# Performance work log

Measured on AMD Instinct MI355X. Metric: run time of the kernel, lower is better.

Reference implementation:

```python
import jax, jax.numpy as jnp
import numpy as np

B = 32768
INPUT_DIM = 128
MAX_DIM = 1024          # max_dynamic_reservoir_dim (pre-allocated)
ACTIVE = 512            # current_reservoir_size (runtime-active prefix)
LEAK = 0.2              # initial leak_rate
THRESH = 0.5            # initial spike_threshold


def setup_inputs() -> dict:
    key = jax.random.key(0)
    k = jax.random.split(key, 5)
    inputs = jax.random.normal(k[0], (B, INPUT_DIM), dtype=jnp.float32)
    prev_state = jax.random.normal(k[1], (B, MAX_DIM), dtype=jnp.float32)
    # Weights initialized like tf RandomNormal(stddev=0.1), pre-allocated to max dim
    W_res = 0.1 * jax.random.normal(k[2], (MAX_DIM, MAX_DIM), dtype=jnp.float32)
    W_in = 0.1 * jax.random.normal(k[3], (MAX_DIM, INPUT_DIM), dtype=jnp.float32)
    W_gate = 0.1 * jax.random.normal(k[4], (3 * MAX_DIM, INPUT_DIM), dtype=jnp.float32)
    # Trainable per-neuron params, initialized to inverse-sigmoid / inverse-softplus of initial values
    leak_rate_param = jnp.full((MAX_DIM,), np.log(LEAK / (1.0 - LEAK)), dtype=jnp.float32)
    spike_threshold_param = jnp.full((MAX_DIM,), np.log(np.expm1(THRESH)), dtype=jnp.float32)
    return {
        'inputs': inputs,
        'prev_state': prev_state,
        'W_res': W_res,
        'W_in': W_in,
        'W_gate': W_gate,
        'leak_rate_param': leak_rate_param,
        'spike_threshold_param': spike_threshold_param,
        'active_size': ACTIVE,
    }


def reference(inputs, prev_state, W_res, W_in, W_gate, leak_rate_param,
              spike_threshold_param, active_size):
    A = active_size
    max_dim = prev_state.shape[1]
    prev = prev_state[:, :A]                                   # [B, A]
    leak = jax.nn.sigmoid(leak_rate_param[:A])                 # [A]
    thr = jax.nn.softplus(spike_threshold_param[:A])           # [A]
    input_part = inputs @ W_in[:A, :].T                        # [B, A]
    reservoir_part = prev @ W_res[:A, :A]                      # [B, A]
    gates = jax.nn.sigmoid(inputs @ W_gate[:3 * A, :].T)       # [B, 3A]
    i_gate, f_gate, o_gate = jnp.split(gates, 3, axis=-1)
    state = (1.0 - leak) * (f_gate * prev) + leak * jnp.tanh(i_gate * (input_part + reservoir_part))
    state = o_gate * state
    # Threshold-triggered spiking reset: subtract threshold where state exceeds it
    state = jnp.where(state > thr, state - thr, state)
    # Pad active state back to the full pre-allocated reservoir width
    return jnp.pad(state, ((0, 0), (0, max_dim - A)))
```

## Files before the change

kernel.cpp:

```cpp
#include <hip/hip_runtime.h>
#include <cmath>

#define NB   32768
#define DIN  128
#define DMAX 1024
#define A    512

typedef _Float16 half8 __attribute__((ext_vector_type(8)));
typedef float f32x4 __attribute__((ext_vector_type(4)));

#define WS_RES_H 0
#define WS_RES_L 262144
#define WS_PAN   524288

__global__ __launch_bounds__(256) void split_weights(
    const float* __restrict__ Wres, const float* __restrict__ Win,
    const float* __restrict__ Wg, _Float16* __restrict__ ws)
{
    int idx = blockIdx.x * 256 + threadIdx.x;
    if (idx < 262144) {
        int k = idx >> 9, j = idx & 511;
        float v = Wres[k * DMAX + j];
        _Float16 h = (_Float16)v;
        _Float16 l = (_Float16)(v - (float)h);
        int off = ((j >> 7) * 16 + (k >> 5)) * 4096 + (j & 127) * 32 + (k & 31);
        ws[WS_RES_H + off] = h;
        ws[WS_RES_L + off] = l;
    } else {
        int r = idx - 262144;
        int p = r >> 16;
        int q = r & 65535;
        int j = q >> 7, k = q & 127;
        float v = (p == 0) ? Win[j * DIN + k]
                           : Wg[((p - 1) * 512 + j) * DIN + k];
        _Float16 h = (_Float16)v;
        _Float16 l = (_Float16)(v - (float)h);
        int off = ((j >> 7) * 4 + (k >> 5)) * 4096 + (j & 127) * 32 + (k & 31);
        ws[WS_PAN + p * 131072 + off] = h;
        ws[WS_PAN + p * 131072 + 65536 + off] = l;
    }
}

__device__ __forceinline__ float sigm(float x) { return 1.0f / (1.0f + expf(-x)); }

__global__ __launch_bounds__(256, 2) void gser_mfma(
    const float* __restrict__ X,
    const float* __restrict__ P,
    const _Float16* __restrict__ ws,
    const float* __restrict__ lrp, const float* __restrict__ stp,
    float* __restrict__ out)
{
    __shared__ _Float16 Ah[128][40], Al[128][40], Bh[128][40], Bl[128][40];

    const int t    = threadIdx.x;
    const int lane = t & 63;
    const int w    = t >> 6;
    const int wm   = w & 1, wn = w >> 1;
    const int quad = lane >> 4, l16 = lane & 15;
    const int jb   = blockIdx.x;
    const int m0   = blockIdx.y * 128;
    const int j0   = jb * 128;

    const int sm = t >> 1;
    const int sk = (t & 1) * 16;

    auto stageA = [&](const float* src, int lda, int k0) {
        const float* p = src + (size_t)sm * lda + k0 + sk;
        float4 f0 = *(const float4*)(p);
        float4 f1 = *(const float4*)(p + 4);
        float4 f2 = *(const float4*)(p + 8);
        float4 f3 = *(const float4*)(p + 12);
        float fv[16] = {f0.x,f0.y,f0.z,f0.w, f1.x,f1.y,f1.z,f1.w,
                        f2.x,f2.y,f2.z,f2.w, f3.x,f3.y,f3.z,f3.w};
        half8 hh0, hh1, ll0, ll1;
#pragma unroll
        for (int i = 0; i < 8; ++i) {
            _Float16 h = (_Float16)fv[i];
            hh0[i] = h; ll0[i] = (_Float16)(fv[i] - (float)h);
        }
#pragma unroll
        for (int i = 0; i < 8; ++i) {
            _Float16 h = (_Float16)fv[8 + i];
            hh1[i] = h; ll1[i] = (_Float16)(fv[8 + i] - (float)h);
        }
        *(half8*)&Ah[sm][sk]     = hh0;
        *(half8*)&Ah[sm][sk + 8] = hh1;
        *(half8*)&Al[sm][sk]     = ll0;
        *(half8*)&Al[sm][sk + 8] = ll1;
    };

    auto stageB = [&](const _Float16* chH, const _Float16* chL) {
#pragma unroll
        for (int r = 0; r < 2; ++r) {
            int s  = t + r * 256;
            int bj = s >> 2, bk = (s & 3) * 8;
            *(half8*)&Bh[bj][bk] = *(const half8*)(chH + s * 8);
            *(half8*)&Bl[bj][bk] = *(const half8*)(chL + s * 8);
        }
    };

    auto mmac = [&](f32x4 (&C)[4][4]) {
        half8 fah[4], fal[4];
#pragma unroll
        for (int ms = 0; ms < 4; ++ms) {
            int row = wm * 64 + ms * 16 + l16;
            fah[ms] = *(const half8*)&Ah[row][quad * 8];
            fal[ms] = *(const half8*)&Al[row][quad * 8];
        }
#pragma unroll
        for (int js = 0; js < 4; ++js) {
            int col = wn * 64 + js * 16 + l16;
            half8 fbh = *(const half8*)&Bh[col][quad * 8];
            half8 fbl = *(const half8*)&Bl[col][quad * 8];
#pragma unroll
            for (int ms = 0; ms < 4; ++ms) {
                C[ms][js] = __builtin_amdgcn_mfma_f32_16x16x32_f16(fah[ms], fbh, C[ms][js], 0, 0, 0);
                C[ms][js] = __builtin_amdgcn_mfma_f32_16x16x32_f16(fah[ms], fbl, C[ms][js], 0, 0, 0);
                C[ms][js] = __builtin_amdgcn_mfma_f32_16x16x32_f16(fal[ms], fbh, C[ms][js], 0, 0, 0);
            }
        }
    };

    f32x4 accS[4][4];
#pragma unroll
    for (int i = 0; i < 4; ++i)
#pragma unroll
        for (int j = 0; j < 4; ++j)
            accS[i][j] = (f32x4){0.f, 0.f, 0.f, 0.f};

    const float* Pblk = P + (size_t)m0 * DMAX;
    for (int kc = 0; kc < 16; ++kc) {
        __syncthreads();
        stageA(Pblk, DMAX, kc * 32);
        const _Float16* ch = ws + WS_RES_H + (size_t)(jb * 16 + kc) * 4096;
        const _Float16* cl = ws + WS_RES_L + (size_t)(jb * 16 + kc) * 4096;
        stageB(ch, cl);
        __syncthreads();
        mmac(accS);
    }

    const float* Xblk = X + (size_t)m0 * DIN;
    for (int kc = 0; kc < 4; ++kc) {
        __syncthreads();
        stageA(Xblk, DIN, kc * 32);
        const _Float16* base = ws + WS_PAN + 0 * 131072;
        stageB(base + (size_t)(jb * 4 + kc) * 4096,
               base + 65536 + (size_t)(jb * 4 + kc) * 4096);
        __syncthreads();
        mmac(accS);
    }

    f32x4 accG[4][4];

#pragma unroll
    for (int i = 0; i < 4; ++i)
#pragma unroll
        for (int j = 0; j < 4; ++j)
            accG[i][j] = (f32x4){0.f, 0.f, 0.f, 0.f};
    for (int kc = 0; kc < 4; ++kc) {
        __syncthreads();
        stageA(Xblk, DIN, kc * 32);
        const _Float16* base = ws + WS_PAN + 1 * 131072;
        stageB(base + (size_t)(jb * 4 + kc) * 4096,
               base + 65536 + (size_t)(jb * 4 + kc) * 4096);
        __syncthreads();
        mmac(accG);
    }
#pragma unroll
    for (int ms = 0; ms < 4; ++ms)
#pragma unroll
        for (int js = 0; js < 4; ++js)
#pragma unroll
            for (int r = 0; r < 4; ++r)
                accS[ms][js][r] = tanhf(sigm(accG[ms][js][r]) * accS[ms][js][r]);

#pragma unroll
    for (int i = 0; i < 4; ++i)
#pragma unroll
        for (int j = 0; j < 4; ++j)
            accG[i][j] = (f32x4){0.f, 0.f, 0.f, 0.f};
    for (int kc = 0; kc < 4; ++kc) {
        __syncthreads();
        stageA(Xblk, DIN, kc * 32);
        const _Float16* base = ws + WS_PAN + 2 * 131072;
        stageB(base + (size_t)(jb * 4 + kc) * 4096,
               base + 65536 + (size_t)(jb * 4 + kc) * 4096);
        __syncthreads();
        mmac(accG);
    }
    {
        float lk[4];
#pragma unroll
        for (int js = 0; js < 4; ++js)
            lk[js] = sigm(lrp[j0 + wn * 64 + js * 16 + l16]);
#pragma unroll
        for (int ms = 0; ms < 4; ++ms)
#pragma unroll
            for (int r = 0; r < 4; ++r) {
                int row = m0 + wm * 64 + ms * 16 + quad * 4 + r;
#pragma unroll
                for (int js = 0; js < 4; ++js) {
                    int col = j0 + wn * 64 + js * 16 + l16;
                    float pv = P[(size_t)row * DMAX + col];
                    float fg = sigm(accG[ms][js][r]);
                    accS[ms][js][r] = (1.0f - lk[js]) * (fg * pv) + lk[js] * accS[ms][js][r];
                }
            }
    }

#pragma unroll
    for (int i = 0; i < 4; ++i)
#pragma unroll
        for (int j = 0; j < 4; ++j)
            accG[i][j] = (f32x4){0.f, 0.f, 0.f, 0.f};
    for (int kc = 0; kc < 4; ++kc) {
        __syncthreads();
        stageA(Xblk, DIN, kc * 32);
        const _Float16* base = ws + WS_PAN + 3 * 131072;
        stageB(base + (size_t)(jb * 4 + kc) * 4096,
               base + 65536 + (size_t)(jb * 4 + kc) * 4096);
        __syncthreads();
        mmac(accG);
    }
    {
        float thr[4];
#pragma unroll
        for (int js = 0; js < 4; ++js)
            thr[js] = log1pf(expf(stp[j0 + wn * 64 + js * 16 + l16]));
#pragma unroll
        for (int ms = 0; ms < 4; ++ms)
#pragma unroll
            for (int r = 0; r < 4; ++r) {
                int row = m0 + wm * 64 + ms * 16 + quad * 4 + r;
#pragma unroll
                for (int js = 0; js < 4; ++js) {
                    int col = j0 + wn * 64 + js * 16 + l16;
                    float st = sigm(accG[ms][js][r]) * accS[ms][js][r];
                    st = (st > thr[js]) ? (st - thr[js]) : st;
                    out[(size_t)row * DMAX + col] = st;
                }
            }
    }

#pragma unroll
    for (int i = 0; i < 16; ++i) {
        int s  = t + i * 256;
        int rr = s >> 5, c4 = s & 31;
        *(float4*)(out + (size_t)(m0 + rr) * DMAX + A + jb * 128 + c4 * 4) =
            (float4){0.f, 0.f, 0.f, 0.f};
    }
}

extern "C" void kernel_launch(void* const* d_in, const int* in_sizes, int n_in,
                              void* d_out, int out_size, void* d_ws, size_t ws_size,
                              hipStream_t stream) {
    const float* X    = (const float*)d_in[0];
    const float* P    = (const float*)d_in[1];
    const float* Wres = (const float*)d_in[2];
    const float* Win  = (const float*)d_in[3];
    const float* Wg   = (const float*)d_in[4];
    const float* lrp  = (const float*)d_in[5];
    const float* stp  = (const float*)d_in[6];
    float* out = (float*)d_out;
    _Float16* ws = (_Float16*)d_ws;

    hipLaunchKernelGGL(split_weights, dim3(2048), dim3(256), 0, stream,
                       Wres, Win, Wg, ws);
    hipLaunchKernelGGL(gser_mfma, dim3(4, 256), dim3(256), 0, stream,
                       X, P, ws, lrp, stp, out);
}
```

Baseline: 448.7 us.

## Pre-split activations to swizzled fp16 tiles and stream via global_load_lds double buffering

Adds a prep kernel that converts X and prev_state, along with the weights, into hi/lo fp16 tile layouts with an XOR swizzle in the workspace. A new main kernel then loads those tiles directly into LDS with global_load_lds and a double-buffered pipeline, and remaps blocks so neighbouring ones share tiles in cache. It also switches to fast exp-based sigmoid and tanh. This removes per-block fp32-to-fp16 conversion and register staging in the GEMM loop, at the cost of an extra full pass that reads and writes the activations. The new path runs only when the workspace is large enough; otherwise the old path is kept.

Measured after the change: 507.8 us. 13.2% more time.

```diff
diff --git a/kernel.cpp b/kernel.cpp
--- a/kernel.cpp
+++ b/kernel.cpp
@@ -12,6 +12,14 @@
 #define WS_RES_H 0
 #define WS_RES_L 262144
 #define WS_PAN   524288
+#define WS_X     1048576
+#define WS_X_LD  4194304
+#define WS_P     9437184
+#define WS_P_LD  16777216
+#define WS_NEED_BYTES 85983232ull
+
+#define SWZB(b) ((b) ^ ((((b) >> 6) & 7) << 4))
+__device__ __forceinline__ unsigned swzh(unsigned h) { return h ^ (((h >> 5) & 7u) << 3); }
 
 __global__ __launch_bounds__(256) void split_weights(
     const float* __restrict__ Wres, const float* __restrict__ Win,
@@ -44,8 +52,7 @@
 __device__ __forceinline__ float sigm(float x) { return 1.0f / (1.0f + expf(-x)); }
 
 __global__ __launch_bounds__(256, 2) void gser_mfma(
-    const float* __restrict__ X,
-    const float* __restrict__ P,
+    const float* __restrict__ X, const float* __restrict__ P,
     const _Float16* __restrict__ ws,
     const float* __restrict__ lrp, const float* __restrict__ stp,
     float* __restrict__ out)
@@ -236,6 +243,278 @@
                 for (int js = 0; js < 4; ++js) {
                     int col = j0 + wn * 64 + js * 16 + l16;
                     float st = sigm(accG[ms][js][r]) * accS[ms][js][r];
+                    st = (st > thr[js]) ? (st - thr[js]) : st;
+                    out[(size_t)row * DMAX + col] = st;
+                }
+            }
+    }
+
+#pragma unroll
+    for (int i = 0; i < 16; ++i) {
+        int s  = t + i * 256;
+        int rr = s >> 5, c4 = s & 31;
+        *(float4*)(out + (size_t)(m0 + rr) * DMAX + A + jb * 128 + c4 * 4) =
+            (float4){0.f, 0.f, 0.f, 0.f};
+    }
+}
+
+
+__global__ __launch_bounds__(256) void prep_full(
+    const float* __restrict__ X, const float* __restrict__ P,
+    const float* __restrict__ Wres, const float* __restrict__ Win,
+    const float* __restrict__ Wg, _Float16* __restrict__ ws)
+{
+    const int NRES = 32768;
+    const int NPAN = 32768;
+    const int NX   = 524288;
+    const int NTOT = NRES + NPAN + NX + 2097152;
+    for (int gi = blockIdx.x * 256 + threadIdx.x; gi < NTOT; gi += gridDim.x * 256) {
+        float v[8];
+        size_t dH, dL;
+        if (gi < NRES) {
+            int j = gi & 511, k0 = (gi >> 9) << 3;
+#pragma unroll
+            for (int i = 0; i < 8; ++i) v[i] = Wres[(size_t)(k0 + i) * DMAX + j];
+            unsigned off = (unsigned)((j >> 7) * 16 + (k0 >> 5)) * 4096u
+                         + swzh((unsigned)((j & 127) * 32 + (k0 & 31)));
+            dH = WS_RES_H + off; dL = WS_RES_L + off;
+        } else if (gi < NRES + NPAN) {
+            int r = gi - NRES;
+            int pj = r >> 4, k0 = (r & 15) << 3;
+            int p = pj >> 9, j = pj & 511;
+            const float* s = (p == 0) ? (Win + (size_t)j * DIN + k0)
+                                      : (Wg + (size_t)((p - 1) * 512 + j) * DIN + k0);
+            float4 f0 = *(const float4*)s, f1 = *(const float4*)(s + 4);
+            v[0] = f0.x; v[1] = f0.y; v[2] = f0.z; v[3] = f0.w;
+            v[4] = f1.x; v[5] = f1.y; v[6] = f1.z; v[7] = f1.w;
+            unsigned off = (unsigned)((j >> 7) * 4 + (k0 >> 5)) * 4096u
+                         + swzh((unsigned)((j & 127) * 32 + (k0 & 31)));
+            dH = WS_PAN + (size_t)p * 131072 + off; dL = dH + 65536;
+        } else if (gi < NRES + NPAN + NX) {
+            int r = gi - (NRES + NPAN);
+            int m = r >> 4, k0 = (r & 15) << 3;
+            const float* s = X + (size_t)m * DIN + k0;
+            float4 f0 = *(const float4*)s, f1 = *(const float4*)(s + 4);
+            v[0] = f0.x; v[1] = f0.y; v[2] = f0.z; v[3] = f0.w;
+            v[4] = f1.x; v[5] = f1.y; v[6] = f1.z; v[7] = f1.w;
+            unsigned off = (unsigned)((m >> 7) * 4 + (k0 >> 5)) * 4096u
+                         + swzh((unsigned)((m & 127) * 32 + (k0 & 31)));
+            dH = WS_X + off; dL = dH + WS_X_LD;
+        } else {
+            int r = gi - (NRES + NPAN + NX);
+            int m = r >> 6, k0 = (r & 63) << 3;
+            const float* s = P + (size_t)m * DMAX + k0;
+            float4 f0 = *(const float4*)s, f1 = *(const float4*)(s + 4);
+            v[0] = f0.x; v[1] = f0.y; v[2] = f0.z; v[3] = f0.w;
+            v[4] = f1.x; v[5] = f1.y; v[6] = f1.z; v[7] = f1.w;
+            unsigned off = (unsigned)((m >> 7) * 16 + (k0 >> 5)) * 4096u
+                         + swzh((unsigned)((m & 127) * 32 + (k0 & 31)));
+            dH = WS_P + off; dL = dH + WS_P_LD;
+        }
+        half8 hh, ll;
+#pragma unroll
+        for (int i = 0; i < 8; ++i) {
+            _Float16 h = (_Float16)v[i];
+            hh[i] = h;
+            ll[i] = (_Float16)(v[i] - (float)h);
+        }
+        *(half8*)(ws + dH) = hh;
+        *(half8*)(ws + dL) = ll;
+    }
+}
+
+__device__ __forceinline__ float fsigm(float x) { return 1.0f / (1.0f + __expf(-x)); }
+__device__ __forceinline__ float ftanh(float x) {
+    float e = __expf(-2.0f * fabsf(x));
+    float t = (1.0f - e) / (1.0f + e);
+    return (x < 0.0f) ? -t : t;
+}
+
+__device__ __forceinline__ void gl16(const _Float16* src, _Float16* dst) {
+    __builtin_amdgcn_global_load_lds(
+        (const __attribute__((address_space(1))) unsigned int*)src,
+        (__attribute__((address_space(3))) unsigned int*)dst, 16, 0, 0);
+}
+
+__global__ __launch_bounds__(256, 2) void gser2(
+    const float* __restrict__ X, const float* __restrict__ P,
+    const _Float16* __restrict__ ws,
+    const float* __restrict__ lrp, const float* __restrict__ stp,
+    float* __restrict__ out)
+{
+    __shared__ _Float16 lds[2][16384];
+
+    const int t    = threadIdx.x;
+    const int lane = t & 63;
+    const int w    = t >> 6;
+    const int wm   = w & 1, wn = w >> 1;
+    const int quad = lane >> 4, l16 = lane & 15;
+
+    const int id = blockIdx.x;
+    const int x8 = id & 7;
+    const int s8 = id >> 3;
+    const int jb = s8 & 3;
+    const int g  = (s8 >> 2) * 8 + x8;
+    const int m0 = g * 128;
+    const int j0 = jb * 128;
+
+    int aOff[4], bOff[4];
+#pragma unroll
+    for (int ms = 0; ms < 4; ++ms) {
+        int b = (wm * 64 + ms * 16 + l16) * 64 + quad * 16;
+        aOff[ms] = SWZB(b);
+    }
+#pragma unroll
+    for (int js = 0; js < 4; ++js) {
+        int b = (wn * 64 + js * 16 + l16) * 64 + quad * 16;
+        bOff[js] = SWZB(b);
+    }
+
+    const int so = w * 512 + lane * 8;
+    const int dd = w * 512;
+
+    auto stage = [&](int buf, int s) {
+        const _Float16 *aB, *bB;
+        unsigned aLd, bLd;
+        if (s < 16) {
+            aB = ws + WS_P + (size_t)(g * 16 + s) * 4096;      aLd = WS_P_LD;
+            bB = ws + WS_RES_H + (size_t)(jb * 16 + s) * 4096; bLd = 262144u;
+        } else {
+            int p = (s - 16) >> 2, kc = s & 3;
+            aB = ws + WS_X + (size_t)(g * 4 + kc) * 4096;      aLd = WS_X_LD;
+            bB = ws + WS_PAN + (size_t)p * 131072 + (size_t)(jb * 4 + kc) * 4096;
+            bLd = 65536u;
+        }
+        _Float16* l = &lds[buf][0];
+#pragma unroll
+        for (int i = 0; i < 2; ++i) {
+            gl16(aB + so + i * 2048,       l + dd + i * 2048);
+            gl16(aB + aLd + so + i * 2048, l + 4096  + dd + i * 2048);
+            gl16(bB + so + i * 2048,       l + 8192  + dd + i * 2048);
+            gl16(bB + bLd + so + i * 2048, l + 12288 + dd + i * 2048);
+        }
+    };
+
+    auto mmac = [&](int buf, f32x4 (&C)[4][4]) {
+        const char* base = (const char*)&lds[buf][0];
+        half8 fah[4], fal[4];
+#pragma unroll
+        for (int ms = 0; ms < 4; ++ms) {
+            fah[ms] = *(const half8*)(base + aOff[ms]);
+            fal[ms] = *(const half8*)(base + 8192 + aOff[ms]);
+        }
+#pragma unroll
+        for (int js = 0; js < 4; ++js) {
+            half8 fbh = *(const half8*)(base + 16384 + bOff[js]);
+            half8 fbl = *(const half8*)(base + 24576 + bOff[js]);
+#pragma unroll
+            for (int ms = 0; ms < 4; ++ms) {
+                C[ms][js] = __builtin_amdgcn_mfma_f32_16x16x32_f16(fah[ms], fbh, C[ms][js], 0, 0, 0);
+                C[ms][js] = __builtin_amdgcn_mfma_f32_16x16x32_f16(fah[ms], fbl, C[ms][js], 0, 0, 0);
+                C[ms][js] = __builtin_amdgcn_mfma_f32_16x16x32_f16(fal[ms], fbh, C[ms][js], 0, 0, 0);
+            }
+        }
+    };
+
+    f32x4 accS[4][4], accG[4][4];
+#pragma unroll
+    for (int i = 0; i < 4; ++i)
+#pragma unroll
+        for (int j = 0; j < 4; ++j)
+            accS[i][j] = (f32x4){0.f, 0.f, 0.f, 0.f};
+
+    int buf = 0;
+    stage(0, 0);
+    __syncthreads();
+
+    for (int s = 0; s < 16; ++s) {
+        stage(buf ^ 1, s + 1);
+        mmac(buf, accS);
+        __syncthreads();
+        buf ^= 1;
+    }
+    for (int s = 16; s < 20; ++s) {
+        stage(buf ^ 1, s + 1);
+        mmac(buf, accS);
+        __syncthreads();
+        buf ^= 1;
+    }
+
+#pragma unroll
+    for (int i = 0; i < 4; ++i)
+#pragma unroll
+        for (int j = 0; j < 4; ++j)
+            accG[i][j] = (f32x4){0.f, 0.f, 0.f, 0.f};
+    for (int s = 20; s < 24; ++s) {
+        stage(buf ^ 1, s + 1);
+        mmac(buf, accG);
+        __syncthreads();
+        buf ^= 1;
+    }
+#pragma unroll
+    for (int ms = 0; ms < 4; ++ms)
+#pragma unroll
+        for (int js = 0; js < 4; ++js)
+#pragma unroll
+            for (int r = 0; r < 4; ++r)
+                accS[ms][js][r] = ftanh(fsigm(accG[ms][js][r]) * accS[ms][js][r]);
+
+#pragma unroll
+    for (int i = 0; i < 4; ++i)
+#pragma unroll
+        for (int j = 0; j < 4; ++j)
+            accG[i][j] = (f32x4){0.f, 0.f, 0.f, 0.f};
+    for (int s = 24; s < 28; ++s) {
+        stage(buf ^ 1, s + 1);
+        mmac(buf, accG);
+        __syncthreads();
+        buf ^= 1;
+    }
+    {
+        float lk[4];
+#pragma unroll
+        for (int js = 0; js < 4; ++js)
+            lk[js] = fsigm(lrp[j0 + wn * 64 + js * 16 + l16]);
+#pragma unroll
+        for (int ms = 0; ms < 4; ++ms)
+#pragma unroll
+            for (int r = 0; r < 4; ++r) {
+                int row = m0 + wm * 64 + ms * 16 + quad * 4 + r;
+#pragma unroll
+                for (int js = 0; js < 4; ++js) {
+                    int col = j0 + wn * 64 + js * 16 + l16;
+                    float pv = P[(size_t)row * DMAX + col];
+                    float fg = fsigm(accG[ms][js][r]);
+                    accS[ms][js][r] = (1.0f - lk[js]) * (fg * pv) + lk[js] * accS[ms][js][r];
+                }
+            }
+    }
+
+#pragma unroll
+    for (int i = 0; i < 4; ++i)
+#pragma unroll
+        for (int j = 0; j < 4; ++j)
+            accG[i][j] = (f32x4){0.f, 0.f, 0.f, 0.f};
+    for (int s = 28; s < 32; ++s) {
+        if (s < 31) stage(buf ^ 1, s + 1);
+        mmac(buf, accG);
+        __syncthreads();
+        buf ^= 1;
+    }
+    {
+        float thr[4];
+#pragma unroll
+        for (int js = 0; js < 4; ++js)
+            thr[js] = log1pf(__expf(stp[j0 + wn * 64 + js * 16 + l16]));
+#pragma unroll
+        for (int ms = 0; ms < 4; ++ms)
+#pragma unroll
+            for (int r = 0; r < 4; ++r) {
+                int row = m0 + wm * 64 + ms * 16 + quad * 4 + r;
+#pragma unroll
+                for (int js = 0; js < 4; ++js) {
+                    int col = j0 + wn * 64 + js * 16 + l16;
+                    float st = fsigm(accG[ms][js][r]) * accS[ms][js][r];
                     st = (st > thr[js]) ? (st - thr[js]) : st;
                     out[(size_t)row * DMAX + col] = st;
                 }
@@ -264,8 +543,15 @@
     float* out = (float*)d_out;
     _Float16* ws = (_Float16*)d_ws;
 
-    hipLaunchKernelGGL(split_weights, dim3(2048), dim3(256), 0, stream,
-                       Wres, Win, Wg, ws);
-    hipLaunchKernelGGL(gser_mfma, dim3(4, 256), dim3(256), 0, stream,
-                       X, P, ws, lrp, stp, out);
-}
+    if (ws_size >= WS_NEED_BYTES) {
+        hipLaunchKernelGGL(prep_full, dim3(10496), dim3(256), 0, stream,
+                           X, P, Wres, Win, Wg, ws);
+        hipLaunchKernelGGL(gser2, dim3(1024), dim3(256), 0, stream,
+                           X, P, ws, lrp, stp, out);
+    } else {
+        hipLaunchKernelGGL(split_weights, dim3(2048), dim3(256), 0, stream,
+                           Wres, Win, Wg, ws);
+        hipLaunchKernelGGL(gser_mfma, dim3(4, 256), dim3(256), 0, stream,
+                           X, P, ws, lrp, stp, out);
+    }
+}
```

## Double-buffer LDS with async global-to-LDS loads, swizzled layout, fast math

Applied to the files above, without the earlier changes.

Moves the main kernel to a double-buffered LDS pipeline. The weight tiles go straight from global memory into LDS with global_load_lds, while the next A tile is loaded into registers and converted during the current MFMA step, leaving one barrier per step. Weights are pre-swizzled in a rewritten prep kernel so LDS fragment reads avoid bank conflicts. Block indices are remapped for L2 locality, and expf/tanhf are replaced with __expf-based approximations. The fast math may lose some accuracy, and the dependence on the swizzle and the async-load layout adds correctness risk.

Measured after the change: 498.5 us. +11.1%, slower.

```diff
diff --git a/kernel.cpp b/kernel.cpp
--- a/kernel.cpp
+++ b/kernel.cpp
@@ -13,105 +13,161 @@
 #define WS_RES_L 262144
 #define WS_PAN   524288
 
-__global__ __launch_bounds__(256) void split_weights(
+#define SWZB(b) ((b) ^ ((((b) >> 6) & 7) << 4))
+__device__ __forceinline__ unsigned swzh(unsigned h) { return h ^ (((h >> 5) & 7u) << 3); }
+
+__device__ __forceinline__ float fsigm(float x) { return 1.0f / (1.0f + __expf(-x)); }
+__device__ __forceinline__ float ftanh(float x) {
+    float e = __expf(-2.0f * fabsf(x));
+    float t = (1.0f - e) / (1.0f + e);
+    return (x < 0.0f) ? -t : t;
+}
+
+__device__ __forceinline__ void gl16(const _Float16* src, _Float16* dst) {
+    __builtin_amdgcn_global_load_lds(
+        (const __attribute__((address_space(1))) unsigned int*)src,
+        (__attribute__((address_space(3))) unsigned int*)dst, 16, 0, 0);
+}
+
+__global__ __launch_bounds__(256) void prep_w(
     const float* __restrict__ Wres, const float* __restrict__ Win,
     const float* __restrict__ Wg, _Float16* __restrict__ ws)
 {
-    int idx = blockIdx.x * 256 + threadIdx.x;
-    if (idx < 262144) {
-        int k = idx >> 9, j = idx & 511;
-        float v = Wres[k * DMAX + j];
-        _Float16 h = (_Float16)v;
-        _Float16 l = (_Float16)(v - (float)h);
-        int off = ((j >> 7) * 16 + (k >> 5)) * 4096 + (j & 127) * 32 + (k & 31);
-        ws[WS_RES_H + off] = h;
-        ws[WS_RES_L + off] = l;
+    int tid = blockIdx.x * 256 + threadIdx.x;
+    float v[32];
+    size_t dH, dL;
+    int j = tid & 127;
+    if (tid < 8192) {
+        int c = tid >> 7;
+        int jbb = c >> 4, kc = c & 15;
+        int col = jbb * 128 + j;
+#pragma unroll
+        for (int i = 0; i < 32; ++i)
+            v[i] = Wres[(size_t)(kc * 32 + i) * DMAX + col];
+        dH = WS_RES_H + (size_t)c * 4096;
+        dL = WS_RES_L + (size_t)c * 4096;
     } else {
-        int r = idx - 262144;
-        int p = r >> 16;
-        int q = r & 65535;
-        int j = q >> 7, k = q & 127;
-        float v = (p == 0) ? Win[j * DIN + k]
-                           : Wg[((p - 1) * 512 + j) * DIN + k];
-        _Float16 h = (_Float16)v;
-        _Float16 l = (_Float16)(v - (float)h);
-        int off = ((j >> 7) * 4 + (k >> 5)) * 4096 + (j & 127) * 32 + (k & 31);
-        ws[WS_PAN + p * 131072 + off] = h;
-        ws[WS_PAN + p * 131072 + 65536 + off] = l;
-    }
-}
-
-__device__ __forceinline__ float sigm(float x) { return 1.0f / (1.0f + expf(-x)); }
-
-__global__ __launch_bounds__(256, 2) void gser_mfma(
+        int r = tid - 8192;
+        int c = r >> 7;
+        int p = c >> 4, cc = c & 15;
+        int jbb = cc >> 2, kc = cc & 3;
+        int row = jbb * 128 + j;
+        const float* s = (p == 0) ? (Win + (size_t)row * DIN + kc * 32)
+                                  : (Wg + (size_t)((p - 1) * 512 + row) * DIN + kc * 32);
+#pragma unroll
+        for (int i = 0; i < 32; ++i) v[i] = s[i];
+        dH = WS_PAN + (size_t)p * 131072 + (size_t)(jbb * 4 + kc) * 4096;
+        dL = dH + 65536;
+    }
+#pragma unroll
+    for (int g = 0; g < 4; ++g) {
+        half8 hh, ll;
+#pragma unroll
+        for (int i = 0; i < 8; ++i) {
+            float x = v[g * 8 + i];
+            _Float16 h = (_Float16)x;
+            hh[i] = h;
+            ll[i] = (_Float16)(x - (float)h);
+        }
+        unsigned ho = swzh((unsigned)(j * 32 + g * 8));
+        *(half8*)(ws + dH + ho) = hh;
+        *(half8*)(ws + dL + ho) = ll;
+    }
+}
+
+__global__ __launch_bounds__(256, 2) void gser3(
     const float* __restrict__ X,
     const float* __restrict__ P,
     const _Float16* __restrict__ ws,
     const float* __restrict__ lrp, const float* __restrict__ stp,
     float* __restrict__ out)
 {
-    __shared__ _Float16 Ah[128][40], Al[128][40], Bh[128][40], Bl[128][40];
+    __shared__ _Float16 lds[2][16384] __attribute__((aligned(16)));
 
     const int t    = threadIdx.x;
     const int lane = t & 63;
     const int w    = t >> 6;
     const int wm   = w & 1, wn = w >> 1;
     const int quad = lane >> 4, l16 = lane & 15;
-    const int jb   = blockIdx.x;
-    const int m0   = blockIdx.y * 128;
-    const int j0   = jb * 128;
+
+    const int id = blockIdx.x;
+    const int x8 = id & 7;
+    const int s8 = id >> 3;
+    const int jb = s8 & 3;
+    const int g  = (s8 >> 2) * 8 + x8;
+    const int m0 = g * 128;
+    const int j0 = jb * 128;
+
+    const float* Pblk = P + (size_t)m0 * DMAX;
+    const float* Xblk = X + (size_t)m0 * DIN;
+
+    int aOff[4], bOff[4];
+#pragma unroll
+    for (int ms = 0; ms < 4; ++ms) {
+        int b = (wm * 64 + ms * 16 + l16) * 64 + quad * 16;
+        aOff[ms] = SWZB(b);
+    }
+#pragma unroll
+    for (int js = 0; js < 4; ++js) {
+        int b = (wn * 64 + js * 16 + l16) * 64 + quad * 16;
+        bOff[js] = SWZB(b);
+    }
 
     const int sm = t >> 1;
     const int sk = (t & 1) * 16;
 
-    auto stageA = [&](const float* src, int lda, int k0) {
-        const float* p = src + (size_t)sm * lda + k0 + sk;
-        float4 f0 = *(const float4*)(p);
-        float4 f1 = *(const float4*)(p + 4);
-        float4 f2 = *(const float4*)(p + 8);
-        float4 f3 = *(const float4*)(p + 12);
-        float fv[16] = {f0.x,f0.y,f0.z,f0.w, f1.x,f1.y,f1.z,f1.w,
-                        f2.x,f2.y,f2.z,f2.w, f3.x,f3.y,f3.z,f3.w};
-        half8 hh0, hh1, ll0, ll1;
+    auto stageB = [&](int buf, int s) {
+        const _Float16 *chH, *chL;
+        if (s < 16) {
+            chH = ws + WS_RES_H + (size_t)(jb * 16 + s) * 4096;
+            chL = ws + WS_RES_L + (size_t)(jb * 16 + s) * 4096;
+        } else {
+            int p = (s - 16) >> 2, kc = s & 3;
+            chH = ws + WS_PAN + (size_t)p * 131072 + (size_t)(jb * 4 + kc) * 4096;
+            chL = chH + 65536;
+        }
+        _Float16* l = &lds[buf][0];
+        gl16(chH + w * 1024 + lane * 8,       l + 8192  + w * 1024);
+        gl16(chH + w * 1024 + 512 + lane * 8, l + 8192  + w * 1024 + 512);
+        gl16(chL + w * 1024 + lane * 8,       l + 12288 + w * 1024);
+        gl16(chL + w * 1024 + 512 + lane * 8, l + 12288 + w * 1024 + 512);
+    };
+
+    auto writeA = [&](int buf, float4 r0, float4 r1, float4 r2, float4 r3) {
+        float fv[16] = {r0.x,r0.y,r0.z,r0.w, r1.x,r1.y,r1.z,r1.w,
+                        r2.x,r2.y,r2.z,r2.w, r3.x,r3.y,r3.z,r3.w};
+        half8 h0, h1, l0, l1;
 #pragma unroll
         for (int i = 0; i < 8; ++i) {
             _Float16 h = (_Float16)fv[i];
-            hh0[i] = h; ll0[i] = (_Float16)(fv[i] - (float)h);
+            h0[i] = h; l0[i] = (_Float16)(fv[i] - (float)h);
         }
 #pragma unroll
         for (int i = 0; i < 8; ++i) {
             _Float16 h = (_Float16)fv[8 + i];
-            hh1[i] = h; ll1[i] = (_Float16)(fv[8 + i] - (float)h);
-        }
-        *(half8*)&Ah[sm][sk]     = hh0;
-        *(half8*)&Ah[sm][sk + 8] = hh1;
-        *(half8*)&Al[sm][sk]     = ll0;
-        *(half8*)&Al[sm][sk + 8] = ll1;
+            h1[i] = h; l1[i] = (_Float16)(fv[8 + i] - (float)h);
+        }
+        char* base = (char*)&lds[buf][0];
+        int a0 = SWZB(sm * 64 + sk * 2);
+        int a1 = SWZB(sm * 64 + sk * 2 + 16);
+        *(half8*)(base + a0) = h0;
+        *(half8*)(base + a1) = h1;
+        *(half8*)(base + 8192 + a0) = l0;
+        *(half8*)(base + 8192 + a1) = l1;
     };
 
-    auto stageB = [&](const _Float16* chH, const _Float16* chL) {
-#pragma unroll
-        for (int r = 0; r < 2; ++r) {
-            int s  = t + r * 256;
-            int bj = s >> 2, bk = (s & 3) * 8;
-            *(half8*)&Bh[bj][bk] = *(const half8*)(chH + s * 8);
-            *(half8*)&Bl[bj][bk] = *(const half8*)(chL + s * 8);
-        }
-    };
-
-    auto mmac = [&](f32x4 (&C)[4][4]) {
+    auto mmac = [&](int buf, f32x4 (&C)[4][4]) {
+        const char* base = (const char*)&lds[buf][0];
         half8 fah[4], fal[4];
 #pragma unroll
         for (int ms = 0; ms < 4; ++ms) {
-            int row = wm * 64 + ms * 16 + l16;
-            fah[ms] = *(const half8*)&Ah[row][quad * 8];
-            fal[ms] = *(const half8*)&Al[row][quad * 8];
+            fah[ms] = *(const half8*)(base + aOff[ms]);
+            fal[ms] = *(const half8*)(base + 8192 + aOff[ms]);
         }
 #pragma unroll
         for (int js = 0; js < 4; ++js) {
-            int col = wn * 64 + js * 16 + l16;
-            half8 fbh = *(const half8*)&Bh[col][quad * 8];
-            half8 fbl = *(const half8*)&Bl[col][quad * 8];
+            half8 fbh = *(const half8*)(base + 16384 + bOff[js]);
+            half8 fbl = *(const half8*)(base + 24576 + bOff[js]);
 #pragma unroll
             for (int ms = 0; ms < 4; ++ms) {
                 C[ms][js] = __builtin_amdgcn_mfma_f32_16x16x32_f16(fah[ms], fbh, C[ms][js], 0, 0, 0);
@@ -121,78 +177,70 @@
         }
     };
 
-    f32x4 accS[4][4];
+    auto krnstep = [&](int s, f32x4 (&acc)[4][4], bool last) {
+        const int bcur = s & 1, bnxt = bcur ^ 1;
+        float4 r0, r1, r2, r3;
+        if (!last) {
+            const int sn = s + 1;
+            const float* srcA = (sn < 16)
+                ? (Pblk + (size_t)sm * DMAX + sn * 32 + sk)
+                : (Xblk + (size_t)sm * DIN + (sn & 3) * 32 + sk);
+            r0 = *(const float4*)(srcA);
+            r1 = *(const float4*)(srcA + 4);
+            r2 = *(const float4*)(srcA + 8);
+            r3 = *(const float4*)(srcA + 12);
+            stageB(bnxt, sn);
+        }
+        mmac(bcur, acc);
+        if (!last) writeA(bnxt, r0, r1, r2, r3);
+        __syncthreads();
+    };
+
+    f32x4 accS[4][4], accG[4][4];
 #pragma unroll
     for (int i = 0; i < 4; ++i)
 #pragma unroll
         for (int j = 0; j < 4; ++j)
             accS[i][j] = (f32x4){0.f, 0.f, 0.f, 0.f};
 
-    const float* Pblk = P + (size_t)m0 * DMAX;
-    for (int kc = 0; kc < 16; ++kc) {
+    {
+        const float* srcA = Pblk + (size_t)sm * DMAX + sk;
+        float4 r0 = *(const float4*)(srcA);
+        float4 r1 = *(const float4*)(srcA + 4);
+        float4 r2 = *(const float4*)(srcA + 8);
+        float4 r3 = *(const float4*)(srcA + 12);
+        stageB(0, 0);
+        writeA(0, r0, r1, r2, r3);
         __syncthreads();
-        stageA(Pblk, DMAX, kc * 32);
-        const _Float16* ch = ws + WS_RES_H + (size_t)(jb * 16 + kc) * 4096;
-        const _Float16* cl = ws + WS_RES_L + (size_t)(jb * 16 + kc) * 4096;
-        stageB(ch, cl);
-        __syncthreads();
-        mmac(accS);
-    }
-
-    const float* Xblk = X + (size_t)m0 * DIN;
-    for (int kc = 0; kc < 4; ++kc) {
-        __syncthreads();
-        stageA(Xblk, DIN, kc * 32);
-        const _Float16* base = ws + WS_PAN + 0 * 131072;
-        stageB(base + (size_t)(jb * 4 + kc) * 4096,
-               base + 65536 + (size_t)(jb * 4 + kc) * 4096);
-        __syncthreads();
-        mmac(accS);
-    }
-
-    f32x4 accG[4][4];
+    }
+
+    for (int s = 0; s < 20; ++s) krnstep(s, accS, false);
 
 #pragma unroll
     for (int i = 0; i < 4; ++i)
 #pragma unroll
         for (int j = 0; j < 4; ++j)
             accG[i][j] = (f32x4){0.f, 0.f, 0.f, 0.f};
-    for (int kc = 0; kc < 4; ++kc) {
-        __syncthreads();
-        stageA(Xblk, DIN, kc * 32);
-        const _Float16* base = ws + WS_PAN + 1 * 131072;
-        stageB(base + (size_t)(jb * 4 + kc) * 4096,
-               base + 65536 + (size_t)(jb * 4 + kc) * 4096);
-        __syncthreads();
-        mmac(accG);
-    }
+    for (int s = 20; s < 24; ++s) krnstep(s, accG, false);
 #pragma unroll
     for (int ms = 0; ms < 4; ++ms)
 #pragma unroll
         for (int js = 0; js < 4; ++js)
 #pragma unroll
             for (int r = 0; r < 4; ++r)
-                accS[ms][js][r] = tanhf(sigm(accG[ms][js][r]) * accS[ms][js][r]);
+                accS[ms][js][r] = ftanh(fsigm(accG[ms][js][r]) * accS[ms][js][r]);
 
 #pragma unroll
     for (int i = 0; i < 4; ++i)
 #pragma unroll
         for (int j = 0; j < 4; ++j)
             accG[i][j] = (f32x4){0.f, 0.f, 0.f, 0.f};
-    for (int kc = 0; kc < 4; ++kc) {
-        __syncthreads();
-        stageA(Xblk, DIN, kc * 32);
-        const _Float16* base = ws + WS_PAN + 2 * 131072;
-        stageB(base + (size_t)(jb * 4 + kc) * 4096,
-               base + 65536 + (size_t)(jb * 4 + kc) * 4096);
-        __syncthreads();
-        mmac(accG);
-    }
+    for (int s = 24; s < 28; ++s) krnstep(s, accG, false);
     {
         float lk[4];
 #pragma unroll
         for (int js = 0; js < 4; ++js)
-            lk[js] = sigm(lrp[j0 + wn * 64 + js * 16 + l16]);
+            lk[js] = fsigm(lrp[j0 + wn * 64 + js * 16 + l16]);
 #pragma unroll
         for (int ms = 0; ms < 4; ++ms)
 #pragma unroll
@@ -202,7 +250,7 @@
                 for (int js = 0; js < 4; ++js) {
                     int col = j0 + wn * 64 + js * 16 + l16;
                     float pv = P[(size_t)row * DMAX + col];
-                    float fg = sigm(accG[ms][js][r]);
+                    float fg = fsigm(accG[ms][js][r]);
                     accS[ms][js][r] = (1.0f - lk[js]) * (fg * pv) + lk[js] * accS[ms][js][r];
                 }
             }
@@ -213,20 +261,13 @@
 #pragma unroll
         for (int j = 0; j < 4; ++j)
             accG[i][j] = (f32x4){0.f, 0.f, 0.f, 0.f};
-    for (int kc = 0; kc < 4; ++kc) {
-        __syncthreads();
-        stageA(Xblk, DIN, kc * 32);
-        const _Float16* base = ws + WS_PAN + 3 * 131072;
-        stageB(base + (size_t)(jb * 4 + kc) * 4096,
-               base + 65536 + (size_t)(jb * 4 + kc) * 4096);
-        __syncthreads();
-        mmac(accG);
-    }
+    for (int s = 28; s < 31; ++s) krnstep(s, accG, false);
+    krnstep(31, accG, true);
     {
         float thr[4];
 #pragma unroll
         for (int js = 0; js < 4; ++js)
-            thr[js] = log1pf(expf(stp[j0 + wn * 64 + js * 16 + l16]));
+            thr[js] = log1pf(__expf(stp[j0 + wn * 64 + js * 16 + l16]));
 #pragma unroll
         for (int ms = 0; ms < 4; ++ms)
 #pragma unroll
@@ -235,7 +276,7 @@
 #pragma unroll
                 for (int js = 0; js < 4; ++js) {
                     int col = j0 + wn * 64 + js * 16 + l16;
-                    float st = sigm(accG[ms][js][r]) * accS[ms][js][r];
+                    float st = fsigm(accG[ms][js][r]) * accS[ms][js][r];
                     st = (st > thr[js]) ? (st - thr[js]) : st;
                     out[(size_t)row * DMAX + col] = st;
                 }
@@ -264,8 +305,8 @@
     float* out = (float*)d_out;
     _Float16* ws = (_Float16*)d_ws;
 
-    hipLaunchKernelGGL(split_weights, dim3(2048), dim3(256), 0, stream,
+    hipLaunchKernelGGL(prep_w, dim3(64), dim3(256), 0, stream,
                        Wres, Win, Wg, ws);
-    hipLaunchKernelGGL(gser_mfma, dim3(4, 256), dim3(256), 0, stream,
+    hipLaunchKernelGGL(gser3, dim3(1024), dim3(256), 0, stream,
                        X, P, ws, lrp, stp, out);
 }
```
